# Optimization experiments

Hardware: AMD Instinct MI355X
Metric: run time of the kernel (lower is better)

The kernel has to match this reference:

```python
import jax, jax.numpy as jnp
import numpy as np

B, T, NOBJ = 512, 20, 36
D, V, EMB, E = 2048, 10000, 300, 512
HM, HO = 1024, 256


def setup_inputs() -> dict:
    key = jax.random.key(0)
    ks = jax.random.split(key, 20)
    s = 0.05
    return {
        "obj_enc": jax.random.normal(ks[0], (B, NOBJ, D), jnp.float32),
        "x": jax.random.randint(ks[1], (B, T), 0, V, dtype=jnp.int32),
        "q_means_mask": jax.random.normal(ks[2], (B, T, E), jnp.float32),
        "q_logs_mask": jax.random.normal(ks[3], (B, T, E), jnp.float32) * 0.1,
        "q_z_mask": jax.random.normal(ks[4], (B, T, E), jnp.float32),
        "q_means_obj": jax.random.normal(ks[5], (B, T, E), jnp.float32),
        "q_logs_obj": jax.random.normal(ks[6], (B, T, E), jnp.float32) * 0.1,
        "q_z_obj": jax.random.normal(ks[7], (B, T, E), jnp.float32),
        # learned parameters
        "emd_W": jax.random.normal(ks[8], (V, EMB), jnp.float32) * s,
        "W_ih_m": jax.random.normal(ks[9], (4 * HM, D + E + EMB), jnp.float32) * s,
        "W_hh_m": jax.random.normal(ks[10], (4 * HM, HM), jnp.float32) * s,
        "b_m": jax.random.normal(ks[11], (4 * HM,), jnp.float32) * s,
        "W_ih_o": jax.random.normal(ks[12], (4 * HO, D + 2 * E + EMB), jnp.float32) * s,
        "W_hh_o": jax.random.normal(ks[13], (4 * HO, HO), jnp.float32) * s,
        "b_o": jax.random.normal(ks[14], (4 * HO,), jnp.float32) * s,
        "fc_m_W": jax.random.normal(ks[15], (2 * E, HM), jnp.float32) * s,
        "fc_m_b": jax.random.normal(ks[16], (2 * E,), jnp.float32) * s,
        "fc_o_W": jax.random.normal(ks[17], (2 * E, HO), jnp.float32) * s,
        "fc_o_b": jax.random.normal(ks[18], (2 * E,), jnp.float32) * s,
    }


def _lstm_cell(xt, h, c, W_ih, W_hh, b):
    # torch LSTMCell gate order: i, f, g, o
    g = xt @ W_ih.T + h @ W_hh.T + b
    i, f, gg, o = jnp.split(g, 4, axis=-1)
    c = jax.nn.sigmoid(f) * c + jax.nn.sigmoid(i) * jnp.tanh(gg)
    h = jax.nn.sigmoid(o) * jnp.tanh(c)
    return h, c


def _kl(p_means, p_logs, q_means, q_logs):
    return (0.5 * (p_logs - q_logs)
            + (jnp.exp(q_logs) + (q_means - p_means) ** 2) / (2.0 * jnp.exp(p_logs))
            - 0.5)


def reference(obj_enc, x, q_means_mask, q_logs_mask, q_z_mask,
              q_means_obj, q_logs_obj, q_z_obj,
              emd_W, W_ih_m, W_hh_m, b_m, W_ih_o, W_hh_o, b_o,
              fc_m_W, fc_m_b, fc_o_W, fc_o_b):
    bsz = obj_enc.shape[0]
    # masked mean over object regions
    obj_mask = (jnp.sum(jnp.abs(obj_enc), axis=-1) > 0).astype(obj_enc.dtype)  # [B,N]
    meanimfeats = (obj_enc * obj_mask[..., None]).sum(1) / jnp.maximum(obj_mask.sum(1, keepdims=True), 1e-9)  # [B,D]

    seq_mask = ((x != 0) & (x != 2)).astype(jnp.float32)  # [B,T]
    x_emb = emd_W[x]  # [B,T,EMB]

    # teacher-forced previous latents (zeros at t=0)
    z_m_prev = jnp.concatenate([jnp.zeros_like(q_z_mask[:, :1]), q_z_mask[:, :-1]], axis=1)
    z_o_prev = jnp.concatenate([jnp.zeros_like(q_z_obj[:, :1]), q_z_obj[:, :-1]], axis=1)

    xs = (jnp.swapaxes(x_emb, 0, 1), jnp.swapaxes(z_m_prev, 0, 1),
          jnp.swapaxes(q_z_mask, 0, 1), jnp.swapaxes(z_o_prev, 0, 1))  # time-major

    init = (jnp.zeros((bsz, HM), obj_enc.dtype), jnp.zeros((bsz, HM), obj_enc.dtype),
            jnp.zeros((bsz, HO), obj_enc.dtype), jnp.zeros((bsz, HO), obj_enc.dtype))

    def step(carry, ins):
        h_m, c_m, h_o, c_o = carry
        xt, zmp, zmc, zop = ins
        h_m, c_m = _lstm_cell(jnp.concatenate([zmp, xt, meanimfeats], -1), h_m, c_m, W_ih_m, W_hh_m, b_m)
        out_m = h_m @ fc_m_W.T + fc_m_b  # [B,2E]
        h_o, c_o = _lstm_cell(jnp.concatenate([zmc, zop, xt, meanimfeats], -1), h_o, c_o, W_ih_o, W_hh_o, b_o)
        out_o = h_o @ fc_o_W.T + fc_o_b  # [B,2E]
        return (h_m, c_m, h_o, c_o), (out_m, out_o)

    _, (outs_m, outs_o) = jax.lax.scan(step, init, xs)  # [T,B,2E]
    outs_m = jnp.swapaxes(outs_m, 0, 1)  # [B,T,2E]
    outs_o = jnp.swapaxes(outs_o, 0, 1)

    p_means_mask, p_logs_mask = outs_m[..., :E], outs_m[..., E:]
    p_means_obj, p_logs_obj = outs_o[..., :E], outs_o[..., E:]

    kl_mask = (_kl(p_means_mask, p_logs_mask, q_means_mask, q_logs_mask).sum(-1) * seq_mask).sum(-1)
    kl_obj = (_kl(p_means_obj, p_logs_obj, q_means_obj, q_logs_obj).sum(-1) * seq_mask).sum(-1)
    return kl_mask + kl_obj  # [B]
```

## Files before the change

kernel.cpp:

```cpp
#include <hip/hip_runtime.h>

#define Bz 512
#define Tz 20
#define NOBJz 36
#define Dz 2048
#define EMBz 300
#define Ez 512
#define HMz 1024
#define HOz 256
#define KXM 832
#define KXO 1344

typedef short v8s __attribute__((ext_vector_type(8)));
typedef float v4f __attribute__((ext_vector_type(4)));
typedef unsigned short u16;

__device__ __forceinline__ float sigf(float x) { return 1.f / (1.f + __expf(-x)); }
__device__ __forceinline__ float tanhfast(float x) { return 2.f * sigf(2.f * x) - 1.f; }

__device__ __forceinline__ u16 f2bf(float f) {
    union { float f; unsigned u; } v; v.f = f;
    unsigned u = v.u;
    u += 0x7FFFu + ((u >> 16) & 1u);
    return (u16)(u >> 16);
}
__device__ __forceinline__ float bf2f(u16 h) {
    union { unsigned u; float f; } v; v.u = ((unsigned)h) << 16;
    return v.f;
}


__global__ void obj_mask_kernel(const float* __restrict__ obj_enc, float* __restrict__ mask) {
    int bn = blockIdx.x, lane = threadIdx.x;
    const float* row = obj_enc + (size_t)bn * Dz;
    float s = 0.f;
    for (int d = lane; d < Dz; d += 64) s += fabsf(row[d]);
    for (int off = 32; off > 0; off >>= 1) s += __shfl_down(s, off);
    if (lane == 0) mask[bn] = (s > 0.f) ? 1.f : 0.f;
}

__global__ void meanim_kernel(const float* __restrict__ obj_enc, const float* __restrict__ mask,
                              u16* __restrict__ meanim_bf) {
    int idx = blockIdx.x * 256 + threadIdx.x;
    if (idx >= Bz * Dz) return;
    int b = idx / Dz, d = idx - b * Dz;
    float s = 0.f, cnt = 0.f;
    for (int n = 0; n < NOBJz; ++n) {
        float m = mask[b * NOBJz + n];
        cnt += m;
        s += obj_enc[((size_t)b * NOBJz + n) * Dz + d] * m;
    }
    meanim_bf[idx] = f2bf(s / fmaxf(cnt, 1e-9f));
}

__global__ void convert_pad(u16* __restrict__ dst, const float* __restrict__ src,
                            int rows, int src_cols, int ld_src, int col0, int dst_ld, int permH) {
    int idx = blockIdx.x * 256 + threadIdx.x;
    if (idx >= rows * dst_ld) return;
    int rp = idx / dst_ld, c = idx - rp * dst_ld;
    int n = rp;
    if (permH) { int g = (rp >> 4) & 3, u = (rp >> 6) * 16 + (rp & 15); n = g * permH + u; }
    dst[idx] = (c < src_cols) ? f2bf(src[(size_t)n * ld_src + col0 + c]) : (u16)0;
}

__global__ void bias_perm(float* __restrict__ dst, const float* __restrict__ src, int H) {
    int r = blockIdx.x * 256 + threadIdx.x;
    if (r >= 4 * H) return;
    int g = (r >> 4) & 3, u = (r >> 6) * 16 + (r & 15);
    dst[r] = src[g * H + u];
}

__global__ void assemble_Xm(u16* __restrict__ X, const float* __restrict__ qzm,
                            const int* __restrict__ x, const float* __restrict__ emd) {
    int idx = blockIdx.x * 256 + threadIdx.x;
    if (idx >= Tz * Bz * KXM) return;
    int r = idx / KXM, c = idx - r * KXM;
    int t = r / Bz, b = r - t * Bz;
    float v;
    if (c < Ez)             v = (t > 0) ? qzm[((size_t)b * Tz + (t - 1)) * Ez + c] : 0.f;
    else if (c < Ez + EMBz) { int xv = x[b * Tz + t]; v = emd[(size_t)xv * EMBz + (c - Ez)]; }
    else                    v = 0.f;
    X[idx] = f2bf(v);
}

__global__ void assemble_Xo(u16* __restrict__ X, const float* __restrict__ qzm,
                            const float* __restrict__ qzo, const int* __restrict__ x,
                            const float* __restrict__ emd) {
    int idx = blockIdx.x * 256 + threadIdx.x;
    if (idx >= Tz * Bz * KXO) return;
    int r = idx / KXO, c = idx - r * KXO;
    int t = r / Bz, b = r - t * Bz;
    float v;
    if (c < Ez)                 v = qzm[((size_t)b * Tz + t) * Ez + c];
    else if (c < 2 * Ez)        v = (t > 0) ? qzo[((size_t)b * Tz + (t - 1)) * Ez + (c - Ez)] : 0.f;
    else if (c < 2 * Ez + EMBz) { int xv = x[b * Tz + t]; v = emd[(size_t)xv * EMBz + (c - 2 * Ez)]; }
    else                        v = 0.f;
    X[idx] = f2bf(v);
}


__device__ __forceinline__ void mma128(
    const u16* __restrict__ A, int lda, const u16* __restrict__ W, int ldw, int K,
    int bm, int bn, u16* As, u16* Ws, v4f (&acc)[4][4]) {
    const int tid = threadIdx.x;
    const int lane = tid & 63, w = tid >> 6;
    const int wm = w >> 1, wn = w & 1;
    const int r15 = lane & 15, quad = lane >> 4;
    const int lrow = lane >> 3;
    const int lcol = ((lane & 7) ^ lrow) * 8;
    for (int k0 = 0; k0 < K; k0 += 64) {
        const u16* gA = A + (size_t)bm * lda + k0;
        const u16* gW = W + (size_t)bn * ldw + k0;
#pragma unroll
        for (int c = 0; c < 4; ++c) {
            int chunk = w * 4 + c;
            int row = chunk * 8 + lrow;
            __builtin_amdgcn_global_load_lds(
                (const __attribute__((address_space(1))) unsigned int*)(gA + (size_t)row * lda + lcol),
                (__attribute__((address_space(3))) unsigned int*)(As + chunk * 512), 16, 0, 0);
            __builtin_amdgcn_global_load_lds(
                (const __attribute__((address_space(1))) unsigned int*)(gW + (size_t)row * ldw + lcol),
                (__attribute__((address_space(3))) unsigned int*)(Ws + chunk * 512), 16, 0, 0);
        }
        __syncthreads();
#pragma unroll
        for (int kk = 0; kk < 64; kk += 32) {
            v8s a[4], b[4];
#pragma unroll
            for (int i = 0; i < 4; ++i) {
                int r = wm * 64 + 16 * i + r15;
                a[i] = *(const v8s*)&As[r * 64 + (((kk >> 3) + quad) ^ (r15 & 7)) * 8];
            }
#pragma unroll
            for (int j = 0; j < 4; ++j) {
                int r = wn * 64 + 16 * j + r15;
                b[j] = *(const v8s*)&Ws[r * 64 + (((kk >> 3) + quad) ^ (r15 & 7)) * 8];
            }
#pragma unroll
            for (int i = 0; i < 4; ++i)
#pragma unroll
                for (int j = 0; j < 4; ++j)
                    acc[i][j] = __builtin_amdgcn_mfma_f32_16x16x32_bf16(a[i], b[j], acc[i][j], 0, 0, 0);
        }
        __syncthreads();
    }
}

__global__ __launch_bounds__(256) void gemm128(
    const u16* __restrict__ A, int lda, const u16* __restrict__ W, int ldw,
    void* __restrict__ Cv, int ldc, int K,
    const float* __restrict__ bias, const u16* __restrict__ addR, unsigned addR_mask, int out_bf16) {
    __shared__ u16 As[128 * 64];
    __shared__ u16 Ws[128 * 64];
    v4f acc[4][4] = {};
    const int bm = blockIdx.y * 128, bn = blockIdx.x * 128;
    mma128(A, lda, W, ldw, K, bm, bn, As, Ws, acc);
    const int tid = threadIdx.x, lane = tid & 63, w = tid >> 6;
    const int wm = w >> 1, wn = w & 1, r15 = lane & 15, quad = lane >> 4;
    float* Cf = (float*)Cv;
    u16* Cb = (u16*)Cv;
#pragma unroll
    for (int i = 0; i < 4; ++i)
#pragma unroll
        for (int j = 0; j < 4; ++j) {
            int col = bn + wn * 64 + 16 * j + r15;
            float bv = bias ? bias[col] : 0.f;
#pragma unroll
            for (int r = 0; r < 4; ++r) {
                int row = bm + wm * 64 + 16 * i + quad * 4 + r;
                float v = acc[i][j][r] + bv;
                if (addR) v += bf2f(addR[(size_t)(row & addR_mask) * ldc + col]);
                if (out_bf16) Cb[(size_t)row * ldc + col] = f2bf(v);
                else          Cf[(size_t)row * ldc + col] = v;
            }
        }
}

__global__ __launch_bounds__(256) void step_fused(
    const u16* __restrict__ Hm_prev, const u16* __restrict__ Whh_m, const u16* __restrict__ Gm,
    float* __restrict__ cm, u16* __restrict__ hm,
    const u16* __restrict__ Ho_prev, const u16* __restrict__ Whh_o, const u16* __restrict__ Go,
    float* __restrict__ co, u16* __restrict__ ho) {
    __shared__ u16 As[128 * 64];
    __shared__ u16 Ws[128 * 64];
    v4f acc[4][4] = {};
    const int bx = blockIdx.x;
    const u16 *A, *W, *G;
    float* c;
    u16* h;
    int lda, N4, H, bm, bn, K;
    if (bx < 128) {
        bm = (bx >> 5) * 128; bn = (bx & 31) * 128;
        A = Hm_prev; W = Whh_m; G = Gm; c = cm; h = hm; lda = HMz; N4 = 4 * HMz; H = HMz; K = HMz;
    } else {
        int lx = bx - 128;
        bm = (lx >> 3) * 128; bn = (lx & 7) * 128;
        A = Ho_prev; W = Whh_o; G = Go; c = co; h = ho; lda = HOz; N4 = 4 * HOz; H = HOz; K = HOz;
    }
    mma128(A, lda, W, lda, K, bm, bn, As, Ws, acc);
    const int tid = threadIdx.x, lane = tid & 63, w = tid >> 6;
    const int wm = w >> 1, wn = w & 1, r15 = lane & 15, quad = lane >> 4;
    const int u = ((bn + wn * 64) >> 6) * 16 + r15;
#pragma unroll
    for (int i = 0; i < 4; ++i)
#pragma unroll
        for (int r = 0; r < 4; ++r) {
            int b = bm + wm * 64 + 16 * i + quad * 4 + r;
            size_t gb = (size_t)b * N4 + bn + wn * 64 + r15;
            float gi = acc[i][0][r] + bf2f(G[gb]);
            float gf = acc[i][1][r] + bf2f(G[gb + 16]);
            float gg = acc[i][2][r] + bf2f(G[gb + 32]);
            float go = acc[i][3][r] + bf2f(G[gb + 48]);
            size_t ci = (size_t)b * H + u;
            float cn = sigf(gf) * c[ci] + sigf(gi) * tanhfast(gg);
            c[ci] = cn;
            h[ci] = f2bf(sigf(go) * tanhfast(cn));
        }
}

__global__ void cell0(const u16* __restrict__ Gm, float* __restrict__ cm, u16* __restrict__ hm,
                      const u16* __restrict__ Go, float* __restrict__ co, u16* __restrict__ ho) {
    int idx = blockIdx.x * 256 + threadIdx.x;
    if (idx < Bz * HMz) {
        int b = idx / HMz, u = idx - b * HMz;
        size_t gb = (size_t)b * 4 * HMz + ((u >> 4) * 64 + (u & 15));
        float gi = bf2f(Gm[gb]), gf = bf2f(Gm[gb + 16]), gg = bf2f(Gm[gb + 32]), go = bf2f(Gm[gb + 48]);
        (void)gf;
        float cn = sigf(gi) * tanhfast(gg);
        cm[idx] = cn;
        hm[idx] = f2bf(sigf(go) * tanhfast(cn));
    } else {
        idx -= Bz * HMz;
        if (idx >= Bz * HOz) return;
        int b = idx / HOz, u = idx - b * HOz;
        size_t gb = (size_t)b * 4 * HOz + ((u >> 4) * 64 + (u & 15));
        float gi = bf2f(Go[gb]), gg = bf2f(Go[gb + 32]), go = bf2f(Go[gb + 48]);
        float cn = sigf(gi) * tanhfast(gg);
        co[idx] = cn;
        ho[idx] = f2bf(sigf(go) * tanhfast(cn));
    }
}

__global__ __launch_bounds__(256) void kl_kernel(
    const float* __restrict__ outs_m, const float* __restrict__ outs_o,
    const float* __restrict__ qmm, const float* __restrict__ qlm,
    const float* __restrict__ qmo, const float* __restrict__ qlo,
    const int* __restrict__ x, float* __restrict__ out) {
    int b = blockIdx.x, tid = threadIdx.x;
    float total = 0.f;
    for (int t = 0; t < Tz; ++t) {
        int xv = x[b * Tz + t];
        if (xv == 0 || xv == 2) continue;
        const float* pm = outs_m + ((size_t)t * Bz + b) * 1024;
        const float* po = outs_o + ((size_t)t * Bz + b) * 1024;
        const size_t q = ((size_t)b * Tz + t) * Ez;
        for (int e = tid; e < Ez; e += 256) {
            float pmm = pm[e], plm = pm[Ez + e];
            float dm = qmm[q + e] - pmm;
            total += 0.5f * (plm - qlm[q + e]) + (__expf(qlm[q + e]) + dm * dm) / (2.f * __expf(plm)) - 0.5f;
            float pmo = po[e], plo = po[Ez + e];
            float dn = qmo[q + e] - pmo;
            total += 0.5f * (plo - qlo[q + e]) + (__expf(qlo[q + e]) + dn * dn) / (2.f * __expf(plo)) - 0.5f;
        }
    }
    __shared__ float red[256];
    red[tid] = total;
    __syncthreads();
    for (int s = 128; s > 0; s >>= 1) {
        if (tid < s) red[tid] += red[tid + s];
        __syncthreads();
    }
    if (tid == 0) out[b] = red[0];
}

extern "C" void kernel_launch(void* const* d_in, const int* in_sizes, int n_in,
                              void* d_out, int out_size, void* d_ws, size_t ws_size,
                              hipStream_t stream) {
    const float* obj_enc = (const float*)d_in[0];
    const int*   x       = (const int*)d_in[1];
    const float* qmm     = (const float*)d_in[2];
    const float* qlm     = (const float*)d_in[3];
    const float* qzm     = (const float*)d_in[4];
    const float* qmo     = (const float*)d_in[5];
    const float* qlo     = (const float*)d_in[6];
    const float* qzo     = (const float*)d_in[7];
    const float* emd     = (const float*)d_in[8];
    const float* W_ih_m  = (const float*)d_in[9];
    const float* W_hh_m  = (const float*)d_in[10];
    const float* b_m     = (const float*)d_in[11];
    const float* W_ih_o  = (const float*)d_in[12];
    const float* W_hh_o  = (const float*)d_in[13];
    const float* b_o     = (const float*)d_in[14];
    const float* fc_m_W  = (const float*)d_in[15];
    const float* fc_m_b  = (const float*)d_in[16];
    const float* fc_o_W  = (const float*)d_in[17];
    const float* fc_o_b  = (const float*)d_in[18];
    float* out = (float*)d_out;

    char* base = (char*)d_ws;
    size_t off = 0;
    auto alloc = [&](size_t bytes) { char* r = base + off; off += (bytes + 255) & ~(size_t)255; return r; };
    float* mask     = (float*)alloc((size_t)Bz * NOBJz * 4);
    u16* meanim_bf  = (u16*)alloc((size_t)Bz * Dz * 2);
    u16* Whh_m_bf   = (u16*)alloc((size_t)4 * HMz * HMz * 2);
    u16* Whh_o_bf   = (u16*)alloc((size_t)4 * HOz * HOz * 2);
    u16* Winp_m_bf  = (u16*)alloc((size_t)4 * HMz * KXM * 2);
    u16* Winp_o_bf  = (u16*)alloc((size_t)4 * HOz * KXO * 2);
    u16* Wmean_m_bf = (u16*)alloc((size_t)4 * HMz * Dz * 2);
    u16* Wmean_o_bf = (u16*)alloc((size_t)4 * HOz * Dz * 2);
    u16* Wfc_m_bf   = (u16*)alloc((size_t)1024 * HMz * 2);
    u16* Wfc_o_bf   = (u16*)alloc((size_t)1024 * HOz * 2);
    float* b_m_p    = (float*)alloc((size_t)4 * HMz * 4);
    float* b_o_p    = (float*)alloc((size_t)4 * HOz * 4);
    u16* Xin_m      = (u16*)alloc((size_t)Tz * Bz * KXM * 2);
    u16* Xin_o      = (u16*)alloc((size_t)Tz * Bz * KXO * 2);
    u16* const_m_bf = (u16*)alloc((size_t)Bz * 4 * HMz * 2);
    u16* const_o_bf = (u16*)alloc((size_t)Bz * 4 * HOz * 2);
    u16* Ginp_m_bf  = (u16*)alloc((size_t)Tz * Bz * 4 * HMz * 2);
    u16* Ginp_o_bf  = (u16*)alloc((size_t)Tz * Bz * 4 * HOz * 2);
    float* c_m      = (float*)alloc((size_t)Bz * HMz * 4);
    float* c_o      = (float*)alloc((size_t)Bz * HOz * 4);
    u16* H_m        = (u16*)alloc((size_t)Tz * Bz * HMz * 2);
    u16* H_o        = (u16*)alloc((size_t)Tz * Bz * HOz * 2);
    float* outs_m = (float*)Ginp_m_bf;
    float* outs_o = outs_m + (size_t)Tz * Bz * 1024;

    const int TB = Tz * Bz;

    obj_mask_kernel<<<Bz * NOBJz, 64, 0, stream>>>(obj_enc, mask);
    meanim_kernel<<<(Bz * Dz + 255) / 256, 256, 0, stream>>>(obj_enc, mask, meanim_bf);
    assemble_Xm<<<(TB * KXM + 255) / 256, 256, 0, stream>>>(Xin_m, qzm, x, emd);
    assemble_Xo<<<(TB * KXO + 255) / 256, 256, 0, stream>>>(Xin_o, qzm, qzo, x, emd);

    convert_pad<<<(4 * HMz * HMz + 255) / 256, 256, 0, stream>>>(Whh_m_bf, W_hh_m, 4 * HMz, HMz, HMz, 0, HMz, HMz);
    convert_pad<<<(4 * HOz * HOz + 255) / 256, 256, 0, stream>>>(Whh_o_bf, W_hh_o, 4 * HOz, HOz, HOz, 0, HOz, HOz);
    convert_pad<<<(4 * HMz * KXM + 255) / 256, 256, 0, stream>>>(Winp_m_bf, W_ih_m, 4 * HMz, Ez + EMBz, 2860, 0, KXM, HMz);
    convert_pad<<<(4 * HOz * KXO + 255) / 256, 256, 0, stream>>>(Winp_o_bf, W_ih_o, 4 * HOz, 2 * Ez + EMBz, 3372, 0, KXO, HOz);
    convert_pad<<<(4 * HMz * Dz + 255) / 256, 256, 0, stream>>>(Wmean_m_bf, W_ih_m, 4 * HMz, Dz, 2860, Ez + EMBz, Dz, HMz);
    convert_pad<<<(4 * HOz * Dz + 255) / 256, 256, 0, stream>>>(Wmean_o_bf, W_ih_o, 4 * HOz, Dz, 3372, 2 * Ez + EMBz, Dz, HOz);
    convert_pad<<<(1024 * HMz + 255) / 256, 256, 0, stream>>>(Wfc_m_bf, fc_m_W, 1024, HMz, HMz, 0, HMz, 0);
    convert_pad<<<(1024 * HOz + 255) / 256, 256, 0, stream>>>(Wfc_o_bf, fc_o_W, 1024, HOz, HOz, 0, HOz, 0);
    bias_perm<<<(4 * HMz + 255) / 256, 256, 0, stream>>>(b_m_p, b_m, HMz);
    bias_perm<<<(4 * HOz + 255) / 256, 256, 0, stream>>>(b_o_p, b_o, HOz);

    gemm128<<<dim3(4 * HMz / 128, Bz / 128), 256, 0, stream>>>(
        meanim_bf, Dz, Wmean_m_bf, Dz, const_m_bf, 4 * HMz, Dz, b_m_p, nullptr, 0u, 1);
    gemm128<<<dim3(4 * HOz / 128, Bz / 128), 256, 0, stream>>>(
        meanim_bf, Dz, Wmean_o_bf, Dz, const_o_bf, 4 * HOz, Dz, b_o_p, nullptr, 0u, 1);

    gemm128<<<dim3(4 * HMz / 128, TB / 128), 256, 0, stream>>>(
        Xin_m, KXM, Winp_m_bf, KXM, Ginp_m_bf, 4 * HMz, KXM, nullptr, const_m_bf, (unsigned)(Bz - 1), 1);
    gemm128<<<dim3(4 * HOz / 128, TB / 128), 256, 0, stream>>>(
        Xin_o, KXO, Winp_o_bf, KXO, Ginp_o_bf, 4 * HOz, KXO, nullptr, const_o_bf, (unsigned)(Bz - 1), 1);

    cell0<<<(Bz * (HMz + HOz) + 255) / 256, 256, 0, stream>>>(
        Ginp_m_bf, c_m, H_m, Ginp_o_bf, c_o, H_o);

    for (int t = 1; t < Tz; ++t) {
        step_fused<<<160, 256, 0, stream>>>(
            H_m + (size_t)(t - 1) * Bz * HMz, Whh_m_bf, Ginp_m_bf + (size_t)t * Bz * 4 * HMz,
            c_m, H_m + (size_t)t * Bz * HMz,
            H_o + (size_t)(t - 1) * Bz * HOz, Whh_o_bf, Ginp_o_bf + (size_t)t * Bz * 4 * HOz,
            c_o, H_o + (size_t)t * Bz * HOz);
    }

    gemm128<<<dim3(1024 / 128, TB / 128), 256, 0, stream>>>(
        H_m, HMz, Wfc_m_bf, HMz, outs_m, 1024, HMz, fc_m_b, nullptr, 0u, 0);
    gemm128<<<dim3(1024 / 128, TB / 128), 256, 0, stream>>>(
        H_o, HOz, Wfc_o_bf, HOz, outs_o, 1024, HOz, fc_o_b, nullptr, 0u, 0);

    kl_kernel<<<Bz, 256, 0, stream>>>(outs_m, outs_o, qmm, qlm, qmo, qlo, x, out);
}
```

Before: 1.339 ms.

## Double-buffer GEMM LDS tiles and fuse object mask with mean-image kernel

Changes the shared GEMM main loop to double-buffer LDS tiles, issuing the async global-to-LDS loads for the next K tile before the MFMAs on the current one. This removes the per-iteration barrier that sat between each load and its compute. It also merges the object-mask and mean-image kernels into one per-batch kernel. The fused kernel keeps the mask in shared memory, saving a launch and the mask round trip through global memory. LDS use doubles to 64KB per block, which may lower occupancy in the step kernel that runs every timestep.

```diff
diff --git a/kernel.cpp b/kernel.cpp
--- a/kernel.cpp
+++ b/kernel.cpp
@@ -30,27 +30,30 @@
 }
 
 
-__global__ void obj_mask_kernel(const float* __restrict__ obj_enc, float* __restrict__ mask) {
-    int bn = blockIdx.x, lane = threadIdx.x;
-    const float* row = obj_enc + (size_t)bn * Dz;
-    float s = 0.f;
-    for (int d = lane; d < Dz; d += 64) s += fabsf(row[d]);
-    for (int off = 32; off > 0; off >>= 1) s += __shfl_down(s, off);
-    if (lane == 0) mask[bn] = (s > 0.f) ? 1.f : 0.f;
-}
-
-__global__ void meanim_kernel(const float* __restrict__ obj_enc, const float* __restrict__ mask,
-                              u16* __restrict__ meanim_bf) {
-    int idx = blockIdx.x * 256 + threadIdx.x;
-    if (idx >= Bz * Dz) return;
-    int b = idx / Dz, d = idx - b * Dz;
-    float s = 0.f, cnt = 0.f;
-    for (int n = 0; n < NOBJz; ++n) {
-        float m = mask[b * NOBJz + n];
-        cnt += m;
-        s += obj_enc[((size_t)b * NOBJz + n) * Dz + d] * m;
-    }
-    meanim_bf[idx] = f2bf(s / fmaxf(cnt, 1e-9f));
+__global__ __launch_bounds__(256) void meanim_fused(const float* __restrict__ obj_enc,
+                                                    u16* __restrict__ meanim_bf) {
+    const int b = blockIdx.x;
+    const int tid = threadIdx.x, lane = tid & 63, w = tid >> 6;
+    __shared__ float mask_s[NOBJz];
+    for (int n = w; n < NOBJz; n += 4) {
+        const float* row = obj_enc + ((size_t)b * NOBJz + n) * Dz;
+        float s = 0.f;
+        for (int d = lane; d < Dz; d += 64) s += fabsf(row[d]);
+        for (int off = 32; off > 0; off >>= 1) s += __shfl_down(s, off);
+        if (lane == 0) mask_s[n] = (s > 0.f) ? 1.f : 0.f;
+    }
+    __syncthreads();
+    float cnt = 0.f;
+#pragma unroll
+    for (int n = 0; n < NOBJz; ++n) cnt += mask_s[n];
+    const float inv = 1.f / fmaxf(cnt, 1e-9f);
+    for (int d = tid; d < Dz; d += 256) {
+        float s = 0.f;
+#pragma unroll 4
+        for (int n = 0; n < NOBJz; ++n)
+            s += obj_enc[((size_t)b * NOBJz + n) * Dz + d] * mask_s[n];
+        meanim_bf[(size_t)b * Dz + d] = f2bf(s * inv);
+    }
 }
 
 __global__ void convert_pad(u16* __restrict__ dst, const float* __restrict__ src,
@@ -99,6 +102,25 @@
 }
 
 
+#define TILE_E (128 * 64)
+
+__device__ __forceinline__ void stage128(const u16* __restrict__ gA, int lda,
+                                         const u16* __restrict__ gW, int ldw,
+                                         u16* __restrict__ As, u16* __restrict__ Ws,
+                                         int w, int lrow, int lcol) {
+#pragma unroll
+    for (int c = 0; c < 4; ++c) {
+        int chunk = w * 4 + c;
+        int row = chunk * 8 + lrow;
+        __builtin_amdgcn_global_load_lds(
+            (const __attribute__((address_space(1))) unsigned int*)(gA + (size_t)row * lda + lcol),
+            (__attribute__((address_space(3))) unsigned int*)(As + chunk * 512), 16, 0, 0);
+        __builtin_amdgcn_global_load_lds(
+            (const __attribute__((address_space(1))) unsigned int*)(gW + (size_t)row * ldw + lcol),
+            (__attribute__((address_space(3))) unsigned int*)(Ws + chunk * 512), 16, 0, 0);
+    }
+}
+
 __device__ __forceinline__ void mma128(
     const u16* __restrict__ A, int lda, const u16* __restrict__ W, int ldw, int K,
     int bm, int bn, u16* As, u16* Ws, v4f (&acc)[4][4]) {
@@ -108,33 +130,29 @@
     const int r15 = lane & 15, quad = lane >> 4;
     const int lrow = lane >> 3;
     const int lcol = ((lane & 7) ^ lrow) * 8;
+    const u16* gA = A + (size_t)bm * lda;
+    const u16* gW = W + (size_t)bn * ldw;
+    stage128(gA, lda, gW, ldw, As, Ws, w, lrow, lcol);
+    __syncthreads();
+    int cur = 0;
     for (int k0 = 0; k0 < K; k0 += 64) {
-        const u16* gA = A + (size_t)bm * lda + k0;
-        const u16* gW = W + (size_t)bn * ldw + k0;
-#pragma unroll
-        for (int c = 0; c < 4; ++c) {
-            int chunk = w * 4 + c;
-            int row = chunk * 8 + lrow;
-            __builtin_amdgcn_global_load_lds(
-                (const __attribute__((address_space(1))) unsigned int*)(gA + (size_t)row * lda + lcol),
-                (__attribute__((address_space(3))) unsigned int*)(As + chunk * 512), 16, 0, 0);
-            __builtin_amdgcn_global_load_lds(
-                (const __attribute__((address_space(1))) unsigned int*)(gW + (size_t)row * ldw + lcol),
-                (__attribute__((address_space(3))) unsigned int*)(Ws + chunk * 512), 16, 0, 0);
-        }
-        __syncthreads();
+        if (k0 + 64 < K)
+            stage128(gA + k0 + 64, lda, gW + k0 + 64, ldw,
+                     As + (cur ^ 1) * TILE_E, Ws + (cur ^ 1) * TILE_E, w, lrow, lcol);
+        const u16* Asc = As + cur * TILE_E;
+        const u16* Wsc = Ws + cur * TILE_E;
 #pragma unroll
         for (int kk = 0; kk < 64; kk += 32) {
             v8s a[4], b[4];
 #pragma unroll
             for (int i = 0; i < 4; ++i) {
                 int r = wm * 64 + 16 * i + r15;
-                a[i] = *(const v8s*)&As[r * 64 + (((kk >> 3) + quad) ^ (r15 & 7)) * 8];
+                a[i] = *(const v8s*)&Asc[r * 64 + (((kk >> 3) + quad) ^ (r15 & 7)) * 8];
             }
 #pragma unroll
             for (int j = 0; j < 4; ++j) {
                 int r = wn * 64 + 16 * j + r15;
-                b[j] = *(const v8s*)&Ws[r * 64 + (((kk >> 3) + quad) ^ (r15 & 7)) * 8];
+                b[j] = *(const v8s*)&Wsc[r * 64 + (((kk >> 3) + quad) ^ (r15 & 7)) * 8];
             }
 #pragma unroll
             for (int i = 0; i < 4; ++i)
@@ -143,6 +161,7 @@
                     acc[i][j] = __builtin_amdgcn_mfma_f32_16x16x32_bf16(a[i], b[j], acc[i][j], 0, 0, 0);
         }
         __syncthreads();
+        cur ^= 1;
     }
 }
 
@@ -150,8 +169,8 @@
     const u16* __restrict__ A, int lda, const u16* __restrict__ W, int ldw,
     void* __restrict__ Cv, int ldc, int K,
     const float* __restrict__ bias, const u16* __restrict__ addR, unsigned addR_mask, int out_bf16) {
-    __shared__ u16 As[128 * 64];
-    __shared__ u16 Ws[128 * 64];
+    __shared__ u16 As[2 * TILE_E];
+    __shared__ u16 Ws[2 * TILE_E];
     v4f acc[4][4] = {};
     const int bm = blockIdx.y * 128, bn = blockIdx.x * 128;
     mma128(A, lda, W, ldw, K, bm, bn, As, Ws, acc);
@@ -181,8 +200,8 @@
     float* __restrict__ cm, u16* __restrict__ hm,
     const u16* __restrict__ Ho_prev, const u16* __restrict__ Whh_o, const u16* __restrict__ Go,
     float* __restrict__ co, u16* __restrict__ ho) {
-    __shared__ u16 As[128 * 64];
-    __shared__ u16 Ws[128 * 64];
+    __shared__ u16 As[2 * TILE_E];
+    __shared__ u16 Ws[2 * TILE_E];
     v4f acc[4][4] = {};
     const int bx = blockIdx.x;
     const u16 *A, *W, *G;
@@ -300,7 +319,6 @@
     char* base = (char*)d_ws;
     size_t off = 0;
     auto alloc = [&](size_t bytes) { char* r = base + off; off += (bytes + 255) & ~(size_t)255; return r; };
-    float* mask     = (float*)alloc((size_t)Bz * NOBJz * 4);
     u16* meanim_bf  = (u16*)alloc((size_t)Bz * Dz * 2);
     u16* Whh_m_bf   = (u16*)alloc((size_t)4 * HMz * HMz * 2);
     u16* Whh_o_bf   = (u16*)alloc((size_t)4 * HOz * HOz * 2);
@@ -327,8 +345,7 @@
 
     const int TB = Tz * Bz;
 
-    obj_mask_kernel<<<Bz * NOBJz, 64, 0, stream>>>(obj_enc, mask);
-    meanim_kernel<<<(Bz * Dz + 255) / 256, 256, 0, stream>>>(obj_enc, mask, meanim_bf);
+    meanim_fused<<<Bz, 256, 0, stream>>>(obj_enc, meanim_bf);
     assemble_Xm<<<(TB * KXM + 255) / 256, 256, 0, stream>>>(Xin_m, qzm, x, emd);
     assemble_Xo<<<(TB * KXO + 255) / 256, 256, 0, stream>>>(Xin_o, qzm, qzo, x, emd);
 
```

New measurement: 1.424 ms. +6.3%, slower.
